# Optimization experiments

Hardware: AMD Instinct MI355X
Metric: run time of the kernel (lower is better)

The kernel has to match this reference:

```python
import jax, jax.numpy as jnp
import numpy as np

N, A, C = 4096, 512, 100


def setup_inputs() -> dict:
    key = jax.random.key(0)
    k1, k2, k3 = jax.random.split(key, 3)
    features = jax.random.normal(k1, (N, A), dtype=jnp.float32)
    y_s = jax.random.normal(k2, (N, C), dtype=jnp.float32)
    labels = jax.random.randint(k3, (N,), 0, C, dtype=jnp.int64)
    CoVariance = jnp.zeros((C, A, A), dtype=jnp.float32)
    Ave = jnp.zeros((C, A), dtype=jnp.float32)
    Amount = jnp.zeros((C,), dtype=jnp.float32)
    return {"features": features, "y_s": y_s, "CoVariance": CoVariance,
            "Ave": Ave, "Amount": Amount, "labels": labels}


def reference(features, y_s, CoVariance, Ave, Amount, labels):
    n, a = features.shape
    c = Ave.shape[0]
    dt = features.dtype

    onehot = jax.nn.one_hot(labels, c, dtype=dt)            # [N, C]
    counts = onehot.sum(axis=0)                             # [C]
    counts_safe = jnp.where(counts == 0, 1.0, counts)       # Amount_CxA==0 -> 1

    # per-class mean: ave_CxA [C, A]
    sum_feats = onehot.T @ features                          # [C, A]
    ave_CxA = sum_feats / counts_safe[:, None]

    # centered features w.r.t. own-class mean; masked per-class copies
    centered = features - ave_CxA[labels]                    # [N, A]
    masked = onehot.T[:, :, None] * centered[None, :, :]     # [C, N, A]
    # per-class scatter of outer products (equals torch bmm over zero-padded rows)
    var_temp = jnp.einsum('cna,nb->cab', masked, centered) / counts_safe[:, None, None]

    # mixing weights; NaN (0/0) -> 0
    denom = counts + Amount                                  # [C]
    w = jnp.where(denom > 0, counts / denom, 0.0)            # [C]

    ave_old = jax.lax.stop_gradient(Ave)                     # .detach() in torch
    cov_old = jax.lax.stop_gradient(CoVariance)
    diff = ave_old - ave_CxA                                 # [C, A]
    additional_CV = (w * (1.0 - w))[:, None, None] * jnp.einsum('ca,cb->cab', diff, diff)

    new_cov = cov_old * (1.0 - w)[:, None, None] + var_temp * w[:, None, None] + additional_CV
    new_ave = ave_old * (1.0 - w)[:, None] + ave_CxA * w[:, None]
    new_amount = Amount + counts

    logp = jax.nn.log_softmax(y_s, axis=-1)                  # [N, C]
    loss = -jnp.mean(jnp.take_along_axis(logp, labels[:, None], axis=1))

    return loss, new_cov, new_ave, new_amount
```

## Files before the change

### kernel.cpp

```cpp
#include <hip/hip_runtime.h>


#define TM 128
#define KC 16
#define LSTR 132
#define LZ 16

typedef float nf4 __attribute__((ext_vector_type(4)));

__global__ __launch_bounds__(1024) void prep_kernel(
    const int* __restrict__ labels, const float* __restrict__ Amount,
    int* __restrict__ offsets, int* __restrict__ idx_sorted,
    float* __restrict__ w_arr, float* __restrict__ inv_cs,
    float* __restrict__ amount_out, float* __restrict__ out_loss0, int N, int C) {
    __shared__ int hist[1024];
    __shared__ int offs[1025];
    __shared__ int cur[1024];
    const int tid = threadIdx.x;
    for (int c = tid; c < C; c += 1024) { hist[c] = 0; cur[c] = 0; }
    __syncthreads();
    for (int i = tid; i < N; i += 1024) atomicAdd(&hist[labels[i]], 1);
    __syncthreads();
    if (tid == 0) {
        int o = 0;
        for (int c = 0; c < C; ++c) { offs[c] = o; o += hist[c]; }
        offs[C] = o;
    }
    __syncthreads();
    for (int c = tid; c < C; c += 1024) {
        float cf = (float)hist[c];
        float cs = cf > 0.f ? cf : 1.f;
        inv_cs[c] = 1.f / cs;
        float am = Amount[c];
        float dn = cf + am;
        w_arr[c] = dn > 0.f ? cf / dn : 0.f;
        amount_out[c] = am + cf;
        offsets[c] = offs[c];
    }
    if (tid == 0) { offsets[C] = offs[C]; out_loss0[0] = 0.f; }
    for (int i = tid; i < N; i += 1024) {
        int c = labels[i];
        int p = atomicAdd(&cur[c], 1);
        idx_sorted[offs[c] + p] = i;
    }
}

__global__ __launch_bounds__(256) void cov_kernel(
    const float* __restrict__ feats, const float* __restrict__ cov_in,
    const float* __restrict__ Ave_in, const float* __restrict__ y_s,
    const int* __restrict__ labels,
    const int* __restrict__ idx_sorted, const int* __restrict__ offsets,
    const float* __restrict__ w_arr, const float* __restrict__ inv_cs,
    float* __restrict__ out_cov, float* __restrict__ out_ave,
    float* __restrict__ out_loss0,
    int N, int C, int A, float invN) {

    if ((int)blockIdx.z >= C + LZ) {
        __shared__ int idxs[256];
        const int nxy = gridDim.x * gridDim.y;
        const int bid = ((int)blockIdx.z - C - LZ) * nxy
                        + blockIdx.y * gridDim.x + blockIdx.x;
        if (bid >= C) return;
        const int c = bid;
        const int tid = threadIdx.x;
        const int base = offsets[c];
        const int nc = offsets[c + 1] - base;
        const float w = w_arr[c];
        const float ic = inv_cs[c];
        for (int c0 = 0; c0 < A; c0 += 512) {
            const int colA = c0 + tid;
            const int colB = c0 + 256 + tid;
            float s0 = 0.f, s1 = 0.f;
            for (int i0 = 0; i0 < nc; i0 += 256) {
                int chunk = min(256, nc - i0);
                __syncthreads();
                if (tid < chunk) idxs[tid] = idx_sorted[base + i0 + tid];
                __syncthreads();
                int j = 0;
                for (; j + 3 < chunk; j += 4) {
                    const float* f0 = feats + (size_t)idxs[j] * A;
                    const float* f1 = feats + (size_t)idxs[j + 1] * A;
                    const float* f2 = feats + (size_t)idxs[j + 2] * A;
                    const float* f3 = feats + (size_t)idxs[j + 3] * A;
                    if (colA < A) s0 += f0[colA] + f1[colA] + f2[colA] + f3[colA];
                    if (colB < A) s1 += f0[colB] + f1[colB] + f2[colB] + f3[colB];
                }
                for (; j < chunk; ++j) {
                    const float* fr = feats + (size_t)idxs[j] * A;
                    if (colA < A) s0 += fr[colA];
                    if (colB < A) s1 += fr[colB];
                }
            }
            if (colA < A)
                out_ave[(size_t)c * A + colA] =
                    Ave_in[(size_t)c * A + colA] * (1.f - w) + (s0 * ic) * w;
            if (colB < A)
                out_ave[(size_t)c * A + colB] =
                    Ave_in[(size_t)c * A + colB] * (1.f - w) + (s1 * ic) * w;
        }
        return;
    }

    if ((int)blockIdx.z >= C) {
        __shared__ float bsum[4];
        const int lane = threadIdx.x & 63;
        const int wv = threadIdx.x >> 6;
        const int bxy = blockIdx.y * gridDim.x + blockIdx.x;
        const int bid = (blockIdx.z - C) * (gridDim.x * gridDim.y) + bxy;
        const int nwaves = LZ * gridDim.x * gridDim.y * 4;
        const int gw = bid * 4 + wv;
        float wsum = 0.f;
        for (int r = gw; r < N; r += nwaves) {
            const float* row = y_s + (size_t)r * C;
            float m = -1e30f;
            for (int col = lane; col < C; col += 64) m = fmaxf(m, row[col]);
            #pragma unroll
            for (int off = 32; off > 0; off >>= 1) m = fmaxf(m, __shfl_xor(m, off));
            float se = 0.f;
            for (int col = lane; col < C; col += 64) se += __expf(row[col] - m);
            #pragma unroll
            for (int off = 32; off > 0; off >>= 1) se += __shfl_xor(se, off);
            if (lane == 0) wsum += -(row[labels[r]] - m - __logf(se));
        }
        if (lane == 0) bsum[wv] = wsum;
        __syncthreads();
        if (threadIdx.x == 0)
            atomicAdd(out_loss0, (bsum[0] + bsum[1] + bsum[2] + bsum[3]) * invN);
        return;
    }

    const int c  = blockIdx.z;
    const int a0 = blockIdx.y * TM;
    const int b0 = blockIdx.x * TM;
    const int tid = threadIdx.x;

    __shared__ float Xa[KC][LSTR];
    __shared__ float Xb[KC][LSTR];
    __shared__ float muA[TM], muB[TM], dA[TM], dB[TM];

    const float w   = w_arr[c];
    const float omw = 1.f - w;
    const float s   = inv_cs[c] * w;
    const float aw  = w * omw;
    const size_t cbase = (size_t)c * A * A;
    const int ty = tid >> 4, tx = tid & 15;

    if (s > 0.f) {
        const int base = offsets[c];
        const int nc = offsets[c + 1] - base;
        const int li = ty;
        const int cg = tx * 4;
        const int nchunks = (nc + KC - 1) / KC;

        float4 v0, v1, v2, v3;
        {
            v0 = make_float4(0.f, 0.f, 0.f, 0.f); v1 = v0; v2 = v0; v3 = v0;
            if (li < nc) {
                int row = idx_sorted[base + li];
                const float* fr = feats + (size_t)row * A;
                v0 = *reinterpret_cast<const float4*>(fr + a0 + cg);
                v1 = *reinterpret_cast<const float4*>(fr + a0 + cg + 64);
                v2 = *reinterpret_cast<const float4*>(fr + b0 + cg);
                v3 = *reinterpret_cast<const float4*>(fr + b0 + cg + 64);
            }
        }

        float4 sA0 = make_float4(0.f, 0.f, 0.f, 0.f), sA1 = sA0, sB0 = sA0, sB1 = sA0;

        float acc[2][4][2][4] = {};
        if (omw != 0.f) {
            const float sc = omw / s;
            #pragma unroll
            for (int ri = 0; ri < 2; ++ri)
                #pragma unroll
                for (int i = 0; i < 4; ++i) {
                    const size_t rowo = cbase + (size_t)(a0 + ri * 64 + ty * 4 + i) * A + b0;
                    #pragma unroll
                    for (int ci = 0; ci < 2; ++ci) {
                        float4 co = *reinterpret_cast<const float4*>(&cov_in[rowo + ci * 64 + tx * 4]);
                        acc[ri][i][ci][0] = co.x * sc;
                        acc[ri][i][ci][1] = co.y * sc;
                        acc[ri][i][ci][2] = co.z * sc;
                        acc[ri][i][ci][3] = co.w * sc;
                    }
                }
        }

        for (int ch = 0; ch < nchunks; ++ch) {
            __syncthreads();
            *reinterpret_cast<float4*>(&Xa[li][cg])      = v0;
            *reinterpret_cast<float4*>(&Xa[li][cg + 64]) = v1;
            *reinterpret_cast<float4*>(&Xb[li][cg])      = v2;
            *reinterpret_cast<float4*>(&Xb[li][cg + 64]) = v3;
            sA0.x += v0.x; sA0.y += v0.y; sA0.z += v0.z; sA0.w += v0.w;
            sA1.x += v1.x; sA1.y += v1.y; sA1.z += v1.z; sA1.w += v1.w;
            sB0.x += v2.x; sB0.y += v2.y; sB0.z += v2.z; sB0.w += v2.w;
            sB1.x += v3.x; sB1.y += v3.y; sB1.z += v3.z; sB1.w += v3.w;
            __syncthreads();

            if (ch + 1 < nchunks) {
                const int kk = (ch + 1) * KC;
                v0 = make_float4(0.f, 0.f, 0.f, 0.f); v1 = v0; v2 = v0; v3 = v0;
                if (kk + li < nc) {
                    int row = idx_sorted[base + kk + li];
                    const float* fr = feats + (size_t)row * A;
                    v0 = *reinterpret_cast<const float4*>(fr + a0 + cg);
                    v1 = *reinterpret_cast<const float4*>(fr + a0 + cg + 64);
                    v2 = *reinterpret_cast<const float4*>(fr + b0 + cg);
                    v3 = *reinterpret_cast<const float4*>(fr + b0 + cg + 64);
                }
            }

            const int kn = min(KC, nc - ch * KC);
            if (kn == KC) {
                #pragma unroll
                for (int k = 0; k < KC; ++k) {
                    float4 a0v = *reinterpret_cast<const float4*>(&Xa[k][ty * 4]);
                    float4 a1v = *reinterpret_cast<const float4*>(&Xa[k][64 + ty * 4]);
                    float4 b0v = *reinterpret_cast<const float4*>(&Xb[k][tx * 4]);
                    float4 b1v = *reinterpret_cast<const float4*>(&Xb[k][64 + tx * 4]);
                    float af[2][4] = {{a0v.x, a0v.y, a0v.z, a0v.w}, {a1v.x, a1v.y, a1v.z, a1v.w}};
                    float bf[2][4] = {{b0v.x, b0v.y, b0v.z, b0v.w}, {b1v.x, b1v.y, b1v.z, b1v.w}};
                    #pragma unroll
                    for (int ri = 0; ri < 2; ++ri)
                        #pragma unroll
                        for (int i = 0; i < 4; ++i)
                            #pragma unroll
                            for (int ci = 0; ci < 2; ++ci)
                                #pragma unroll
                                for (int j = 0; j < 4; ++j)
                                    acc[ri][i][ci][j] += af[ri][i] * bf[ci][j];
                }
            } else {
                for (int k = 0; k < kn; ++k) {
                    float4 a0v = *reinterpret_cast<const float4*>(&Xa[k][ty * 4]);
                    float4 a1v = *reinterpret_cast<const float4*>(&Xa[k][64 + ty * 4]);
                    float4 b0v = *reinterpret_cast<const float4*>(&Xb[k][tx * 4]);
                    float4 b1v = *reinterpret_cast<const float4*>(&Xb[k][64 + tx * 4]);
                    float af[2][4] = {{a0v.x, a0v.y, a0v.z, a0v.w}, {a1v.x, a1v.y, a1v.z, a1v.w}};
                    float bf[2][4] = {{b0v.x, b0v.y, b0v.z, b0v.w}, {b1v.x, b1v.y, b1v.z, b1v.w}};
                    #pragma unroll
                    for (int ri = 0; ri < 2; ++ri)
                        #pragma unroll
                        for (int i = 0; i < 4; ++i)
                            #pragma unroll
                            for (int ci = 0; ci < 2; ++ci)
                                #pragma unroll
                                for (int j = 0; j < 4; ++j)
                                    acc[ri][i][ci][j] += af[ri][i] * bf[ci][j];
                }
            }
        }

        __syncthreads();
        *reinterpret_cast<float4*>(&Xa[li][cg])      = sA0;
        *reinterpret_cast<float4*>(&Xa[li][cg + 64]) = sA1;
        *reinterpret_cast<float4*>(&Xb[li][cg])      = sB0;
        *reinterpret_cast<float4*>(&Xb[li][cg + 64]) = sB1;
        __syncthreads();
        {
            const int t = tid & 127;
            float sum = 0.f;
            if (tid < 128) {
                #pragma unroll
                for (int r = 0; r < KC; ++r) sum += Xa[r][t];
                float mu = sum * inv_cs[c];
                muA[t] = mu;
                dA[t] = Ave_in[(size_t)c * A + a0 + t] - mu;
            } else {
                #pragma unroll
                for (int r = 0; r < KC; ++r) sum += Xb[r][t];
                float mu = sum * inv_cs[c];
                muB[t] = mu;
                dB[t] = Ave_in[(size_t)c * A + b0 + t] - mu;
            }
        }
        __syncthreads();

        float mb[2][4], db[2][4];
        #pragma unroll
        for (int ci = 0; ci < 2; ++ci)
            #pragma unroll
            for (int j = 0; j < 4; ++j) {
                mb[ci][j] = muB[ci * 64 + tx * 4 + j];
                db[ci][j] = dB[ci * 64 + tx * 4 + j];
            }

        #pragma unroll
        for (int ri = 0; ri < 2; ++ri)
            #pragma unroll
            for (int i = 0; i < 4; ++i) {
                float ma = w  * muA[ri * 64 + ty * 4 + i];
                float da = aw * dA[ri * 64 + ty * 4 + i];
                const size_t rowo = cbase + (size_t)(a0 + ri * 64 + ty * 4 + i) * A + b0;
                #pragma unroll
                for (int ci = 0; ci < 2; ++ci) {
                    nf4 res;
                    res.x = acc[ri][i][ci][0] * s - ma * mb[ci][0] + da * db[ci][0];
                    res.y = acc[ri][i][ci][1] * s - ma * mb[ci][1] + da * db[ci][1];
                    res.z = acc[ri][i][ci][2] * s - ma * mb[ci][2] + da * db[ci][2];
                    res.w = acc[ri][i][ci][3] * s - ma * mb[ci][3] + da * db[ci][3];
                    __builtin_nontemporal_store(res,
                        reinterpret_cast<nf4*>(&out_cov[rowo + ci * 64 + tx * 4]));
                }
            }
    } else {
        for (int t = tid; t < TM * TM / 4; t += 256) {
            const int r = t >> 5;
            const int c4 = (t & 31) * 4;
            const size_t o = cbase + (size_t)(a0 + r) * A + b0 + c4;
            float4 co = *reinterpret_cast<const float4*>(&cov_in[o]);
            nf4 res;
            res.x = co.x * omw; res.y = co.y * omw; res.z = co.z * omw; res.w = co.w * omw;
            __builtin_nontemporal_store(res, reinterpret_cast<nf4*>(&out_cov[o]));
        }
    }
}

extern "C" void kernel_launch(void* const* d_in, const int* in_sizes, int n_in,
                              void* d_out, int out_size, void* d_ws, size_t ws_size,
                              hipStream_t stream) {
    const float* feats  = (const float*)d_in[0];
    const float* y_s    = (const float*)d_in[1];
    const float* cov_in = (const float*)d_in[2];
    const float* Ave_in = (const float*)d_in[3];
    const float* Amount = (const float*)d_in[4];
    const int*   labels = (const int*)d_in[5];

    const int C = in_sizes[4];
    const int N = in_sizes[5];
    const int A = in_sizes[3] / C;

    float* out      = (float*)d_out;
    float* out_loss = out;
    float* out_cov  = out + 1;
    float* out_ave  = out_cov + (size_t)C * A * A;
    float* out_amt  = out_ave + (size_t)C * A;

    char* w8 = (char*)d_ws;
    int* offsets    = (int*)w8;   w8 += (size_t)(C + 1) * sizeof(int);
    int* idx_sorted = (int*)w8;   w8 += (size_t)N * sizeof(int);
    float* w_arr    = (float*)w8; w8 += (size_t)C * sizeof(float);
    float* inv_cs   = (float*)w8; w8 += (size_t)C * sizeof(float);

    prep_kernel<<<1, 1024, 0, stream>>>(labels, Amount, offsets, idx_sorted,
                                        w_arr, inv_cs, out_amt, out_loss, N, C);

    const int nxy = (A / TM) * (A / TM);
    const int AZ = (C + nxy - 1) / nxy;
    dim3 grid(A / TM, A / TM, C + LZ + AZ);
    cov_kernel<<<grid, 256, 0, stream>>>(feats, cov_in, Ave_in, y_s, labels,
                                         idx_sorted, offsets, w_arr, inv_cs,
                                         out_cov, out_ave, out_loss, N, C, A,
                                         1.f / (float)N);
}
```

Measured before the change: 241.2 us.

## Stage feature tiles via direct global-to-LDS loads with double buffering

Replaces the register-staged feature loads and explicit shared-memory stores with global_load_lds direct copies into a double-buffered LDS tile. The next chunk is prefetched while the current one is consumed, which drops one barrier per chunk. Column sums for the class mean are now read back from LDS instead of being accumulated in registers. Launch bounds are tightened to request 4 blocks per CU. The unpadded layout may cause LDS bank conflicts, and tail rows are clamped to nc-1 rather than zero-filled; this relies on the kn loop bound to skip them.

```diff
diff --git a/kernel.cpp b/kernel.cpp
--- a/kernel.cpp
+++ b/kernel.cpp
@@ -3,10 +3,13 @@
 
 #define TM 128
 #define KC 16
-#define LSTR 132
 #define LZ 16
 
 typedef float nf4 __attribute__((ext_vector_type(4)));
+
+#define GLD16(gp, lp) __builtin_amdgcn_global_load_lds( \
+    (const __attribute__((address_space(1))) void*)(gp), \
+    (__attribute__((address_space(3))) void*)(lp), 16, 0, 0)
 
 __global__ __launch_bounds__(1024) void prep_kernel(
     const int* __restrict__ labels, const float* __restrict__ Amount,
@@ -45,7 +48,7 @@
     }
 }
 
-__global__ __launch_bounds__(256) void cov_kernel(
+__global__ __launch_bounds__(256, 4) void cov_kernel(
     const float* __restrict__ feats, const float* __restrict__ cov_in,
     const float* __restrict__ Ave_in, const float* __restrict__ y_s,
     const int* __restrict__ labels,
@@ -134,8 +137,7 @@
     const int b0 = blockIdx.x * TM;
     const int tid = threadIdx.x;
 
-    __shared__ float Xa[KC][LSTR];
-    __shared__ float Xb[KC][LSTR];
+    __shared__ __align__(16) float Xs[2][4][KC][64];
     __shared__ float muA[TM], muB[TM], dA[TM], dB[TM];
 
     const float w   = w_arr[c];
@@ -144,28 +146,28 @@
     const float aw  = w * omw;
     const size_t cbase = (size_t)c * A * A;
     const int ty = tid >> 4, tx = tid & 15;
+    const int ty4 = ty * 4, tx4 = tx * 4;
 
     if (s > 0.f) {
         const int base = offsets[c];
         const int nc = offsets[c + 1] - base;
-        const int li = ty;
-        const int cg = tx * 4;
         const int nchunks = (nc + KC - 1) / KC;
-
-        float4 v0, v1, v2, v3;
-        {
-            v0 = make_float4(0.f, 0.f, 0.f, 0.f); v1 = v0; v2 = v0; v3 = v0;
-            if (li < nc) {
-                int row = idx_sorted[base + li];
-                const float* fr = feats + (size_t)row * A;
-                v0 = *reinterpret_cast<const float4*>(fr + a0 + cg);
-                v1 = *reinterpret_cast<const float4*>(fr + a0 + cg + 64);
-                v2 = *reinterpret_cast<const float4*>(fr + b0 + cg);
-                v3 = *reinterpret_cast<const float4*>(fr + b0 + cg + 64);
-            }
-        }
-
-        float4 sA0 = make_float4(0.f, 0.f, 0.f, 0.f), sA1 = sA0, sB0 = sA0, sB1 = sA0;
+        const int wv = tid >> 6;
+        const int cg4 = tx4;
+
+        auto STAGE = [&](int ch, int b) {
+            int krow = min(ch * KC + (tid >> 4), nc - 1);
+            int row = idx_sorted[base + krow];
+            const float* fr = feats + (size_t)row * A + cg4;
+            float* lA0 = &Xs[b][0][wv * 4][0];
+            float* lA1 = &Xs[b][1][wv * 4][0];
+            float* lB0 = &Xs[b][2][wv * 4][0];
+            float* lB1 = &Xs[b][3][wv * 4][0];
+            GLD16(fr + a0,      lA0);
+            GLD16(fr + a0 + 64, lA1);
+            GLD16(fr + b0,      lB0);
+            GLD16(fr + b0 + 64, lB1);
+        };
 
         float acc[2][4][2][4] = {};
         if (omw != 0.f) {
@@ -174,10 +176,10 @@
             for (int ri = 0; ri < 2; ++ri)
                 #pragma unroll
                 for (int i = 0; i < 4; ++i) {
-                    const size_t rowo = cbase + (size_t)(a0 + ri * 64 + ty * 4 + i) * A + b0;
+                    const size_t rowo = cbase + (size_t)(a0 + ri * 64 + ty4 + i) * A + b0;
                     #pragma unroll
                     for (int ci = 0; ci < 2; ++ci) {
-                        float4 co = *reinterpret_cast<const float4*>(&cov_in[rowo + ci * 64 + tx * 4]);
+                        float4 co = *reinterpret_cast<const float4*>(&cov_in[rowo + ci * 64 + tx4]);
                         acc[ri][i][ci][0] = co.x * sc;
                         acc[ri][i][ci][1] = co.y * sc;
                         acc[ri][i][ci][2] = co.z * sc;
@@ -186,39 +188,25 @@
                 }
         }
 
+        float csum = 0.f;
+        const int cst = tid >> 6;
+        const int csc = tid & 63;
+
+        STAGE(0, 0);
+        __syncthreads();
+
         for (int ch = 0; ch < nchunks; ++ch) {
-            __syncthreads();
-            *reinterpret_cast<float4*>(&Xa[li][cg])      = v0;
-            *reinterpret_cast<float4*>(&Xa[li][cg + 64]) = v1;
-            *reinterpret_cast<float4*>(&Xb[li][cg])      = v2;
-            *reinterpret_cast<float4*>(&Xb[li][cg + 64]) = v3;
-            sA0.x += v0.x; sA0.y += v0.y; sA0.z += v0.z; sA0.w += v0.w;
-            sA1.x += v1.x; sA1.y += v1.y; sA1.z += v1.z; sA1.w += v1.w;
-            sB0.x += v2.x; sB0.y += v2.y; sB0.z += v2.z; sB0.w += v2.w;
-            sB1.x += v3.x; sB1.y += v3.y; sB1.z += v3.z; sB1.w += v3.w;
-            __syncthreads();
-
-            if (ch + 1 < nchunks) {
-                const int kk = (ch + 1) * KC;
-                v0 = make_float4(0.f, 0.f, 0.f, 0.f); v1 = v0; v2 = v0; v3 = v0;
-                if (kk + li < nc) {
-                    int row = idx_sorted[base + kk + li];
-                    const float* fr = feats + (size_t)row * A;
-                    v0 = *reinterpret_cast<const float4*>(fr + a0 + cg);
-                    v1 = *reinterpret_cast<const float4*>(fr + a0 + cg + 64);
-                    v2 = *reinterpret_cast<const float4*>(fr + b0 + cg);
-                    v3 = *reinterpret_cast<const float4*>(fr + b0 + cg + 64);
-                }
-            }
+            const int cur = ch & 1;
+            if (ch + 1 < nchunks) STAGE(ch + 1, cur ^ 1);
 
             const int kn = min(KC, nc - ch * KC);
             if (kn == KC) {
                 #pragma unroll
                 for (int k = 0; k < KC; ++k) {
-                    float4 a0v = *reinterpret_cast<const float4*>(&Xa[k][ty * 4]);
-                    float4 a1v = *reinterpret_cast<const float4*>(&Xa[k][64 + ty * 4]);
-                    float4 b0v = *reinterpret_cast<const float4*>(&Xb[k][tx * 4]);
-                    float4 b1v = *reinterpret_cast<const float4*>(&Xb[k][64 + tx * 4]);
+                    float4 a0v = *reinterpret_cast<const float4*>(&Xs[cur][0][k][ty4]);
+                    float4 a1v = *reinterpret_cast<const float4*>(&Xs[cur][1][k][ty4]);
+                    float4 b0v = *reinterpret_cast<const float4*>(&Xs[cur][2][k][tx4]);
+                    float4 b1v = *reinterpret_cast<const float4*>(&Xs[cur][3][k][tx4]);
                     float af[2][4] = {{a0v.x, a0v.y, a0v.z, a0v.w}, {a1v.x, a1v.y, a1v.z, a1v.w}};
                     float bf[2][4] = {{b0v.x, b0v.y, b0v.z, b0v.w}, {b1v.x, b1v.y, b1v.z, b1v.w}};
                     #pragma unroll
@@ -233,10 +221,10 @@
                 }
             } else {
                 for (int k = 0; k < kn; ++k) {
-                    float4 a0v = *reinterpret_cast<const float4*>(&Xa[k][ty * 4]);
-                    float4 a1v = *reinterpret_cast<const float4*>(&Xa[k][64 + ty * 4]);
-                    float4 b0v = *reinterpret_cast<const float4*>(&Xb[k][tx * 4]);
-                    float4 b1v = *reinterpret_cast<const float4*>(&Xb[k][64 + tx * 4]);
+                    float4 a0v = *reinterpret_cast<const float4*>(&Xs[cur][0][k][ty4]);
+                    float4 a1v = *reinterpret_cast<const float4*>(&Xs[cur][1][k][ty4]);
+                    float4 b0v = *reinterpret_cast<const float4*>(&Xs[cur][2][k][tx4]);
+                    float4 b1v = *reinterpret_cast<const float4*>(&Xs[cur][3][k][tx4]);
                     float af[2][4] = {{a0v.x, a0v.y, a0v.z, a0v.w}, {a1v.x, a1v.y, a1v.z, a1v.w}};
                     float bf[2][4] = {{b0v.x, b0v.y, b0v.z, b0v.w}, {b1v.x, b1v.y, b1v.z, b1v.w}};
                     #pragma unroll
@@ -250,27 +238,21 @@
                                     acc[ri][i][ci][j] += af[ri][i] * bf[ci][j];
                 }
             }
-        }
-
-        __syncthreads();
-        *reinterpret_cast<float4*>(&Xa[li][cg])      = sA0;
-        *reinterpret_cast<float4*>(&Xa[li][cg + 64]) = sA1;
-        *reinterpret_cast<float4*>(&Xb[li][cg])      = sB0;
-        *reinterpret_cast<float4*>(&Xb[li][cg + 64]) = sB1;
-        __syncthreads();
+
+            for (int k = 0; k < kn; ++k) csum += Xs[cur][cst][k][csc];
+
+            __syncthreads();
+        }
+
         {
-            const int t = tid & 127;
-            float sum = 0.f;
+            const float ic = inv_cs[c];
             if (tid < 128) {
-                #pragma unroll
-                for (int r = 0; r < KC; ++r) sum += Xa[r][t];
-                float mu = sum * inv_cs[c];
-                muA[t] = mu;
-                dA[t] = Ave_in[(size_t)c * A + a0 + t] - mu;
+                float mu = csum * ic;
+                muA[tid] = mu;
+                dA[tid] = Ave_in[(size_t)c * A + a0 + tid] - mu;
             } else {
-                #pragma unroll
-                for (int r = 0; r < KC; ++r) sum += Xb[r][t];
-                float mu = sum * inv_cs[c];
+                const int t = tid - 128;
+                float mu = csum * ic;
                 muB[t] = mu;
                 dB[t] = Ave_in[(size_t)c * A + b0 + t] - mu;
             }
@@ -282,17 +264,17 @@
         for (int ci = 0; ci < 2; ++ci)
             #pragma unroll
             for (int j = 0; j < 4; ++j) {
-                mb[ci][j] = muB[ci * 64 + tx * 4 + j];
-                db[ci][j] = dB[ci * 64 + tx * 4 + j];
+                mb[ci][j] = muB[ci * 64 + tx4 + j];
+                db[ci][j] = dB[ci * 64 + tx4 + j];
             }
 
         #pragma unroll
         for (int ri = 0; ri < 2; ++ri)
             #pragma unroll
             for (int i = 0; i < 4; ++i) {
-                float ma = w  * muA[ri * 64 + ty * 4 + i];
-                float da = aw * dA[ri * 64 + ty * 4 + i];
-                const size_t rowo = cbase + (size_t)(a0 + ri * 64 + ty * 4 + i) * A + b0;
+                float ma = w  * muA[ri * 64 + ty4 + i];
+                float da = aw * dA[ri * 64 + ty4 + i];
+                const size_t rowo = cbase + (size_t)(a0 + ri * 64 + ty4 + i) * A + b0;
                 #pragma unroll
                 for (int ci = 0; ci < 2; ++ci) {
                     nf4 res;
@@ -301,7 +283,7 @@
                     res.z = acc[ri][i][ci][2] * s - ma * mb[ci][2] + da * db[ci][2];
                     res.w = acc[ri][i][ci][3] * s - ma * mb[ci][3] + da * db[ci][3];
                     __builtin_nontemporal_store(res,
-                        reinterpret_cast<nf4*>(&out_cov[rowo + ci * 64 + tx * 4]));
+                        reinterpret_cast<nf4*>(&out_cov[rowo + ci * 64 + tx4]));
                 }
             }
     } else {
```

Result: slower. 307.2 us (+27.4%).
